# Kernel tuning notes

Measured on AMD Instinct MI355X. Metric: run time of the kernel, lower is better.

## Reference

```python
import jax, jax.numpy as jnp
import numpy as np

V, H, L, B = 32000, 1024, 2, 64
TEMP = 0.8


def setup_inputs() -> dict:
    key = jax.random.key(0)
    ks = jax.random.split(key, 12)
    sV = 1.0 / np.sqrt(V)
    sH = 1.0 / np.sqrt(H)
    return {
        "x": jax.random.normal(ks[0], (B, V), jnp.float32),
        "hidden_states": jax.random.normal(ks[1], (L, B, H), jnp.float32),
        "cell_states": jax.random.normal(ks[2], (L, B, H), jnp.float32),
        # gate order along axis 1: f, i, o, g
        "Wh": jax.random.uniform(ks[3], (L, 4, H, H), jnp.float32, -sH, sH),
        "bh": jax.random.uniform(ks[4], (L, 4, H), jnp.float32, -sH, sH),
        "Wx0": jax.random.uniform(ks[5], (4, H, V), jnp.float32, -sV, sV),
        "bx0": jax.random.uniform(ks[6], (4, H), jnp.float32, -sV, sV),
        "Wx1": jax.random.uniform(ks[7], (4, H, H), jnp.float32, -sH, sH),
        "bx1": jax.random.uniform(ks[8], (4, H), jnp.float32, -sH, sH),
        "Wdec": jax.random.uniform(ks[9], (V, H), jnp.float32, -sH, sH),
        "bdec": jax.random.uniform(ks[10], (V,), jnp.float32, -sH, sH),
    }


def _lstm_cell(inp, h, c, Wx, bx, Whl, bhl):
    # fused gate pre-activations: [B, 4, H]
    z = (jnp.einsum("ghk,bk->bgh", Wx, inp) + bx[None]
         + jnp.einsum("ghk,bk->bgh", Whl, h) + bhl[None])
    f = jax.nn.sigmoid(z[:, 0])
    i = jax.nn.sigmoid(z[:, 1])
    o = jax.nn.sigmoid(z[:, 2])
    g = jnp.tanh(z[:, 3])
    c_new = f * c + i * g
    out = o * jnp.tanh(c_new)
    return out, c_new


def reference(x, hidden_states, cell_states, Wh, bh, Wx0, bx0, Wx1, bx1, Wdec, bdec):
    wx = [(Wx0, bx0), (Wx1, bx1)]
    outputs, cstates = [], []
    inp = x
    for l in range(L):
        out, c_new = _lstm_cell(inp, hidden_states[l], cell_states[l],
                                wx[l][0], wx[l][1], Wh[l], bh[l])
        outputs.append(out)
        cstates.append(c_new)
        inp = out
    logits = outputs[-1] @ Wdec.T + bdec
    logp = jax.nn.log_softmax(logits / TEMP, axis=-1)
    return logp, jnp.stack(outputs), jnp.stack(cstates)
```

## Files before the change

### kernel.cpp

```cpp
#include <hip/hip_runtime.h>
#include <hip/hip_bf16.h>
#include <cstdint>

#define DI __device__ __forceinline__

typedef __attribute__((ext_vector_type(8))) short short8;
typedef __attribute__((ext_vector_type(4))) float f32x4;
typedef __attribute__((ext_vector_type(4))) int int4v;

DI f32x4 mfma16(short8 a, short8 b, f32x4 c) {
  return __builtin_amdgcn_mfma_f32_16x16x32_bf16(a, b, c, 0, 0, 0);
}

DI uint32_t f2bf(float f) {
  uint32_t u = __float_as_uint(f);
  return (u + 0x7fffu + ((u >> 16) & 1u)) >> 16;
}

DI uint32_t pk2(float a, float b) {
  return f2bf(a) | (f2bf(b) << 16);
}

DI short8 cvt8(float4 a, float4 b) {
  int4v t;
  t.x = (int)pk2(a.x, a.y);
  t.y = (int)pk2(a.z, a.w);
  t.z = (int)pk2(b.x, b.y);
  t.w = (int)pk2(b.z, b.w);
  return __builtin_bit_cast(short8, t);
}

__global__ __launch_bounds__(256) void convert_k(
    const float* __restrict__ x, const float* __restrict__ hs,
    ushort* __restrict__ xb, ushort* __restrict__ hb) {
  const int NX4 = 512000;
  const int NH4 = 32768;
  int i = blockIdx.x * 256 + threadIdx.x;
  if (i < NX4) {
    float4 v = *(const float4*)(x + 4 * (size_t)i);
    uint2 o;
    o.x = pk2(v.x, v.y);
    o.y = pk2(v.z, v.w);
    *(uint2*)(xb + 4 * (size_t)i) = o;
  } else if (i < NX4 + NH4) {
    int j = i - NX4;
    float4 v = *(const float4*)(hs + 4 * (size_t)j);
    uint2 o;
    o.x = pk2(v.x, v.y);
    o.y = pk2(v.z, v.w);
    *(uint2*)(hb + 4 * (size_t)j) = o;
  }
}

__global__ __launch_bounds__(256, 2) void gates_pf(
    const ushort* __restrict__ xb, const ushort* __restrict__ hb,
    const float* __restrict__ Wx0, const float* __restrict__ Wh,
    float* __restrict__ zpart) {
  const int y = blockIdx.y;
  const ushort* A;
  const float* W;
  int ldA, K, steps;
  long kbase;
  if (y < 25) {
    A = xb; ldA = 32000; W = Wx0; K = 32000; steps = 20;
    kbase = (long)y * 1280;
  } else if (y < 27) {
    A = hb; ldA = 1024; W = Wh; K = 1024; steps = 8;
    kbase = (long)(y - 25) * 512;
  } else {
    A = hb + 65536; ldA = 1024; W = Wh + 4194304; K = 1024; steps = 8;
    kbase = (long)(y - 27) * 512;
  }
  const int tid = threadIdx.x;
  const int wv = tid >> 6;
  const int lane = tid & 63;
  const int l15 = lane & 15;
  const int l4 = lane >> 4;
  const int h = blockIdx.x * 64 + wv * 16 + l15;

  const ushort* arow[4];
#pragma unroll
  for (int m = 0; m < 4; ++m)
    arow[m] = A + (size_t)(m * 16 + l15) * ldA + kbase + l4 * 8;
  const float* wrow[4];
#pragma unroll
  for (int g = 0; g < 4; ++g)
    wrow[g] = W + (size_t)(g * 1024 + h) * K + kbase + l4 * 8;

  f32x4 acc[4][4];
#pragma unroll
  for (int g = 0; g < 4; ++g)
#pragma unroll
    for (int m = 0; m < 4; ++m)
      acc[g][m] = f32x4{0.f, 0.f, 0.f, 0.f};

  float4 wt[4][4];
  short8 wb0[4], wb1[4];

#pragma unroll
  for (int g = 0; g < 4; ++g) {
    const float* wp = wrow[g];
    wt[g][0] = *(const float4*)wp;
    wt[g][1] = *(const float4*)(wp + 4);
    wt[g][2] = *(const float4*)(wp + 32);
    wt[g][3] = *(const float4*)(wp + 36);
  }
#pragma unroll
  for (int g = 0; g < 4; ++g) {
    wb0[g] = cvt8(wt[g][0], wt[g][1]);
    wb1[g] = cvt8(wt[g][2], wt[g][3]);
  }

  for (int s = 0; s < steps; ++s) {
    short8 af0[4], af1[4];
#pragma unroll
    for (int m = 0; m < 4; ++m) {
      const ushort* ap = arow[m] + (size_t)s * 64;
      af0[m] = *(const short8*)ap;
      af1[m] = *(const short8*)(ap + 32);
    }
    if (s + 1 < steps) {
#pragma unroll
      for (int g = 0; g < 4; ++g) {
        const float* wp = wrow[g] + (size_t)(s + 1) * 64;
        wt[g][0] = *(const float4*)wp;
        wt[g][1] = *(const float4*)(wp + 4);
        wt[g][2] = *(const float4*)(wp + 32);
        wt[g][3] = *(const float4*)(wp + 36);
      }
    }
#pragma unroll
    for (int g = 0; g < 4; ++g)
#pragma unroll
      for (int m = 0; m < 4; ++m) {
        acc[g][m] = mfma16(af0[m], wb0[g], acc[g][m]);
        acc[g][m] = mfma16(af1[m], wb1[g], acc[g][m]);
      }
    if (s + 1 < steps) {
#pragma unroll
      for (int g = 0; g < 4; ++g) {
        wb0[g] = cvt8(wt[g][0], wt[g][1]);
        wb1[g] = cvt8(wt[g][2], wt[g][3]);
      }
    }
  }

  float* zp = zpart + (size_t)y * 262144 + (size_t)(l4 * 4) * 4096 + h;
#pragma unroll
  for (int g = 0; g < 4; ++g)
#pragma unroll
    for (int m = 0; m < 4; ++m)
#pragma unroll
      for (int r = 0; r < 4; ++r)
        zp[(size_t)(m * 16 + r) * 4096 + g * 1024] = acc[g][m][r];
}

__global__ __launch_bounds__(256) void gates_b16(
    const ushort* __restrict__ A, const float* __restrict__ W,
    float* __restrict__ zbase) {
  const int chunk = blockIdx.y;
  const long kbase = (long)chunk * 64;
  const int tid = threadIdx.x;
  const int wv = tid >> 6;
  const int lane = tid & 63;
  const int l15 = lane & 15;
  const int l4 = lane >> 4;
  const int h = blockIdx.x * 64 + wv * 16 + l15;

  const ushort* arow[4];
#pragma unroll
  for (int m = 0; m < 4; ++m)
    arow[m] = A + (size_t)(m * 16 + l15) * 1024 + kbase + l4 * 8;
  const float* wrow[4];
#pragma unroll
  for (int g = 0; g < 4; ++g)
    wrow[g] = W + (size_t)(g * 1024 + h) * 1024 + kbase + l4 * 8;

  f32x4 acc[4][4];
#pragma unroll
  for (int g = 0; g < 4; ++g)
#pragma unroll
    for (int m = 0; m < 4; ++m)
      acc[g][m] = f32x4{0.f, 0.f, 0.f, 0.f};

#pragma unroll
  for (int s = 0; s < 2; ++s) {
    short8 af[4];
#pragma unroll
    for (int m = 0; m < 4; ++m)
      af[m] = *(const short8*)(arow[m] + (size_t)s * 32);
#pragma unroll
    for (int g = 0; g < 4; ++g) {
      const float* wp = wrow[g] + (size_t)s * 32;
      float4 w0 = *(const float4*)wp;
      float4 w1 = *(const float4*)(wp + 4);
      short8 bfr = cvt8(w0, w1);
#pragma unroll
      for (int m = 0; m < 4; ++m)
        acc[g][m] = mfma16(af[m], bfr, acc[g][m]);
    }
  }

  float* zp = zbase + (size_t)chunk * 262144 + (size_t)(l4 * 4) * 4096 + h;
#pragma unroll
  for (int g = 0; g < 4; ++g)
#pragma unroll
    for (int m = 0; m < 4; ++m)
#pragma unroll
      for (int r = 0; r < 4; ++r)
        zp[(size_t)(m * 16 + r) * 4096 + g * 1024] = acc[g][m][r];
}

__global__ __launch_bounds__(256) void lstm_cell_k(
    const float* __restrict__ zpart, int nslots,
    const float* __restrict__ bx, const float* __restrict__ bhl,
    const float* __restrict__ c_in,
    float* __restrict__ h_out, float* __restrict__ c_out,
    ushort* __restrict__ h_out_b) {
  int idx = blockIdx.x * 256 + threadIdx.x;
  if (idx >= 64 * 1024) return;
  int h = idx & 1023;
  float z0 = bx[h] + bhl[h];
  float z1 = bx[1024 + h] + bhl[1024 + h];
  float z2 = bx[2048 + h] + bhl[2048 + h];
  float z3 = bx[3072 + h] + bhl[3072 + h];
  int b = idx >> 10;
  const float* zp = zpart + (size_t)b * 4096 + h;
  for (int s = 0; s < nslots; ++s) {
    const float* p = zp + (size_t)s * 262144;
    z0 += p[0];
    z1 += p[1024];
    z2 += p[2048];
    z3 += p[3072];
  }
  float f = 1.f / (1.f + expf(-z0));
  float i = 1.f / (1.f + expf(-z1));
  float o = 1.f / (1.f + expf(-z2));
  float g = tanhf(z3);
  float c = f * c_in[idx] + i * g;
  float hv = o * tanhf(c);
  h_out[idx] = hv;
  c_out[idx] = c;
  h_out_b[idx] = (ushort)f2bf(hv);
}

__global__ __launch_bounds__(64) void gemm_dec(
    const ushort* __restrict__ A, const float* __restrict__ W,
    const float* __restrict__ bias, float* __restrict__ logits) {
  const int lane = threadIdx.x;
  const int l15 = lane & 15;
  const int l4 = lane >> 4;
  const int col = blockIdx.x * 16 + l15;

  const ushort* arow[4];
#pragma unroll
  for (int m = 0; m < 4; ++m)
    arow[m] = A + (size_t)(m * 16 + l15) * 1024 + l4 * 8;
  const float* wrow = W + (size_t)col * 1024 + l4 * 8;

  f32x4 acc[4];
#pragma unroll
  for (int m = 0; m < 4; ++m) acc[m] = f32x4{0.f, 0.f, 0.f, 0.f};

  for (int s = 0; s < 32; ++s) {
    short8 af[4];
#pragma unroll
    for (int m = 0; m < 4; ++m)
      af[m] = *(const short8*)(arow[m] + (size_t)s * 32);
    const float* wp = wrow + (size_t)s * 32;
    float4 w0 = *(const float4*)wp;
    float4 w1 = *(const float4*)(wp + 4);
    short8 bfr = cvt8(w0, w1);
#pragma unroll
    for (int m = 0; m < 4; ++m)
      acc[m] = mfma16(af[m], bfr, acc[m]);
  }

  float bv = bias[col];
  float* lp = logits + (size_t)(l4 * 4) * 32000 + col;
#pragma unroll
  for (int m = 0; m < 4; ++m)
#pragma unroll
    for (int r = 0; r < 4; ++r)
      lp[(size_t)(m * 16 + r) * 32000] = acc[m][r] + bv;
}

__global__ __launch_bounds__(256) void softmax_part1(
    const float* __restrict__ logits, float2* __restrict__ ms) {
  const int cx = blockIdx.x;
  const int b = blockIdx.y;
  const int tid = threadIdx.x;
  const int wv = tid >> 6;
  const int lane = tid & 63;
  const float* row = logits + (size_t)b * 32000 + cx * 8000;
  __shared__ float rbuf[4];

  float m = -1e30f;
  for (int i = tid; i < 8000; i += 256) m = fmaxf(m, row[i]);
#pragma unroll
  for (int d = 1; d < 64; d <<= 1) m = fmaxf(m, __shfl_xor(m, d));
  if (lane == 0) rbuf[wv] = m;
  __syncthreads();
  m = fmaxf(fmaxf(rbuf[0], rbuf[1]), fmaxf(rbuf[2], rbuf[3]));
  __syncthreads();

  float sum = 0.f;
  for (int i = tid; i < 8000; i += 256) sum += expf((row[i] - m) * 1.25f);
#pragma unroll
  for (int d = 1; d < 64; d <<= 1) sum += __shfl_xor(sum, d);
  if (lane == 0) rbuf[wv] = sum;
  __syncthreads();
  if (tid == 0) {
    sum = rbuf[0] + rbuf[1] + rbuf[2] + rbuf[3];
    ms[b * 4 + cx] = make_float2(m, sum);
  }
}

__global__ __launch_bounds__(256) void softmax_part2(
    const float* __restrict__ logits, const float2* __restrict__ ms,
    float* __restrict__ logp) {
  const int cx = blockIdx.x;
  const int b = blockIdx.y;
  const int tid = threadIdx.x;

  float2 p0 = ms[b * 4 + 0], p1 = ms[b * 4 + 1];
  float2 p2 = ms[b * 4 + 2], p3 = ms[b * 4 + 3];
  float M = fmaxf(fmaxf(p0.x, p1.x), fmaxf(p2.x, p3.x));
  float S = p0.y * expf((p0.x - M) * 1.25f) + p1.y * expf((p1.x - M) * 1.25f) +
            p2.y * expf((p2.x - M) * 1.25f) + p3.y * expf((p3.x - M) * 1.25f);
  float lse = logf(S);

  const float* row = logits + (size_t)b * 32000 + cx * 4000;
  float* op = logp + (size_t)b * 32000 + cx * 4000;
  for (int i = tid; i < 4000; i += 256)
    op[i] = (row[i] - M) * 1.25f - lse;
}

extern "C" void kernel_launch(void* const* d_in, const int* in_sizes, int n_in,
                              void* d_out, int out_size, void* d_ws, size_t ws_size,
                              hipStream_t stream) {
  const float* x    = (const float*)d_in[0];
  const float* hs   = (const float*)d_in[1];
  const float* cs   = (const float*)d_in[2];
  const float* Wh   = (const float*)d_in[3];
  const float* bh   = (const float*)d_in[4];
  const float* Wx0  = (const float*)d_in[5];
  const float* bx0  = (const float*)d_in[6];
  const float* Wx1  = (const float*)d_in[7];
  const float* bx1  = (const float*)d_in[8];
  const float* Wdec = (const float*)d_in[9];
  const float* bdec = (const float*)d_in[10];

  float* out   = (float*)d_out;
  float* logp  = out;
  float* houts = out + 2048000;
  float* couts = out + 2179072;

  char* ws = (char*)d_ws;
  ushort* xb     = (ushort*)ws;
  ushort* hb     = (ushort*)(ws + 4096000);
  ushort* outb   = (ushort*)(ws + 4358144);
  float*  logits = (float*)(ws + 4620288);
  float2* ms     = (float2*)(ws + 12812288);
  float*  zpart  = (float*)(ws + 12814336);

  convert_k<<<2128, 256, 0, stream>>>(x, hs, xb, hb);

  gates_pf<<<dim3(16, 29), 256, 0, stream>>>(xb, hb, Wx0, Wh, zpart);

  lstm_cell_k<<<256, 256, 0, stream>>>(zpart, 27, bx0, bh, cs,
                                       houts, couts, outb);

  gates_b16<<<dim3(16, 16), 256, 0, stream>>>(
      outb, Wx1, zpart + (size_t)29 * 262144);

  lstm_cell_k<<<256, 256, 0, stream>>>(zpart + (size_t)27 * 262144, 18,
                                       bx1, bh + 4096, cs + 65536,
                                       houts + 65536, couts + 65536,
                                       outb + 65536);

  gemm_dec<<<2000, 64, 0, stream>>>(outb + 65536, Wdec, bdec, logits);

  softmax_part1<<<dim3(4, 64), 256, 0, stream>>>(logits, ms);
  softmax_part2<<<dim3(8, 64), 256, 0, stream>>>(logits, ms, logp);
}
```

Before: 280.6 us.

## Split gate dimension across grid z and double-buffer weight prefetch in gates kernel

```diff
diff --git a/kernel.cpp b/kernel.cpp
--- a/kernel.cpp
+++ b/kernel.cpp
@@ -52,11 +52,12 @@
   }
 }
 
-__global__ __launch_bounds__(256, 2) void gates_pf(
+__global__ __launch_bounds__(256, 2) void gates_pf2(
     const ushort* __restrict__ xb, const ushort* __restrict__ hb,
     const float* __restrict__ Wx0, const float* __restrict__ Wh,
     float* __restrict__ zpart) {
   const int y = blockIdx.y;
+  const int gz = blockIdx.z;
   const ushort* A;
   const float* W;
   int ldA, K, steps;
@@ -82,77 +83,71 @@
 #pragma unroll
   for (int m = 0; m < 4; ++m)
     arow[m] = A + (size_t)(m * 16 + l15) * ldA + kbase + l4 * 8;
-  const float* wrow[4];
-#pragma unroll
-  for (int g = 0; g < 4; ++g)
-    wrow[g] = W + (size_t)(g * 1024 + h) * K + kbase + l4 * 8;
-
-  f32x4 acc[4][4];
-#pragma unroll
-  for (int g = 0; g < 4; ++g)
-#pragma unroll
-    for (int m = 0; m < 4; ++m)
-      acc[g][m] = f32x4{0.f, 0.f, 0.f, 0.f};
-
-  float4 wt[4][4];
-  short8 wb0[4], wb1[4];
-
-#pragma unroll
-  for (int g = 0; g < 4; ++g) {
-    const float* wp = wrow[g];
-    wt[g][0] = *(const float4*)wp;
-    wt[g][1] = *(const float4*)(wp + 4);
-    wt[g][2] = *(const float4*)(wp + 32);
-    wt[g][3] = *(const float4*)(wp + 36);
-  }
-#pragma unroll
-  for (int g = 0; g < 4; ++g) {
-    wb0[g] = cvt8(wt[g][0], wt[g][1]);
-    wb1[g] = cvt8(wt[g][2], wt[g][3]);
-  }
-
-  for (int s = 0; s < steps; ++s) {
-    short8 af0[4], af1[4];
-#pragma unroll
-    for (int m = 0; m < 4; ++m) {
-      const ushort* ap = arow[m] + (size_t)s * 64;
-      af0[m] = *(const short8*)ap;
-      af1[m] = *(const short8*)(ap + 32);
-    }
-    if (s + 1 < steps) {
-#pragma unroll
-      for (int g = 0; g < 4; ++g) {
-        const float* wp = wrow[g] + (size_t)(s + 1) * 64;
-        wt[g][0] = *(const float4*)wp;
-        wt[g][1] = *(const float4*)(wp + 4);
-        wt[g][2] = *(const float4*)(wp + 32);
-        wt[g][3] = *(const float4*)(wp + 36);
-      }
-    }
-#pragma unroll
-    for (int g = 0; g < 4; ++g)
-#pragma unroll
-      for (int m = 0; m < 4; ++m) {
-        acc[g][m] = mfma16(af0[m], wb0[g], acc[g][m]);
-        acc[g][m] = mfma16(af1[m], wb1[g], acc[g][m]);
-      }
-    if (s + 1 < steps) {
-#pragma unroll
-      for (int g = 0; g < 4; ++g) {
-        wb0[g] = cvt8(wt[g][0], wt[g][1]);
-        wb1[g] = cvt8(wt[g][2], wt[g][3]);
-      }
-    }
-  }
-
-  float* zp = zpart + (size_t)y * 262144 + (size_t)(l4 * 4) * 4096 + h;
-#pragma unroll
-  for (int g = 0; g < 4; ++g)
+  const float* wrow[2];
+#pragma unroll
+  for (int gi = 0; gi < 2; ++gi)
+    wrow[gi] = W + (size_t)((gz * 2 + gi) * 1024 + h) * K + kbase + l4 * 8;
+
+  f32x4 acc[2][4];
+#pragma unroll
+  for (int gi = 0; gi < 2; ++gi)
+#pragma unroll
+    for (int m = 0; m < 4; ++m)
+      acc[gi][m] = f32x4{0.f, 0.f, 0.f, 0.f};
+
+  float4 wtA[2][4], wtB[2][4];
+
+#define LOADW(dst, ss)                                             \
+  {                                                                \
+    _Pragma("unroll") for (int gi = 0; gi < 2; ++gi) {             \
+      const float* wp = wrow[gi] + (size_t)(ss) * 64;              \
+      dst[gi][0] = *(const float4*)wp;                             \
+      dst[gi][1] = *(const float4*)(wp + 4);                       \
+      dst[gi][2] = *(const float4*)(wp + 32);                      \
+      dst[gi][3] = *(const float4*)(wp + 36);                      \
+    }                                                              \
+  }
+
+#define SUBITER(wt, ss, reload_s)                                  \
+  {                                                                \
+    short8 af0[4], af1[4];                                         \
+    _Pragma("unroll") for (int m = 0; m < 4; ++m) {                \
+      const ushort* ap = arow[m] + (size_t)(ss) * 64;              \
+      af0[m] = *(const short8*)ap;                                 \
+      af1[m] = *(const short8*)(ap + 32);                          \
+    }                                                              \
+    short8 wb0[2], wb1[2];                                         \
+    _Pragma("unroll") for (int gi = 0; gi < 2; ++gi) {             \
+      wb0[gi] = cvt8(wt[gi][0], wt[gi][1]);                        \
+      wb1[gi] = cvt8(wt[gi][2], wt[gi][3]);                        \
+    }                                                              \
+    if ((reload_s) < steps) LOADW(wt, (reload_s));                 \
+    _Pragma("unroll") for (int gi = 0; gi < 2; ++gi)               \
+        _Pragma("unroll") for (int m = 0; m < 4; ++m) {            \
+      acc[gi][m] = mfma16(af0[m], wb0[gi], acc[gi][m]);            \
+      acc[gi][m] = mfma16(af1[m], wb1[gi], acc[gi][m]);            \
+    }                                                              \
+  }
+
+  LOADW(wtA, 0);
+  LOADW(wtB, 1);
+
+  for (int s = 0; s < steps; s += 2) {
+    SUBITER(wtA, s, s + 2);
+    SUBITER(wtB, s + 1, s + 3);
+  }
+#undef SUBITER
+#undef LOADW
+
+  float* zp = zpart + (size_t)y * 262144 + (size_t)(l4 * 4) * 4096 +
+              (gz * 2) * 1024 + h;
+#pragma unroll
+  for (int gi = 0; gi < 2; ++gi)
 #pragma unroll
     for (int m = 0; m < 4; ++m)
 #pragma unroll
       for (int r = 0; r < 4; ++r)
-        zp[(size_t)(m * 16 + r) * 4096 + g * 1024] = acc[g][m][r];
+        zp[(size_t)(m * 16 + r) * 4096 + gi * 1024] = acc[gi][m][r];
 }
 
 __global__ __launch_bounds__(256) void gates_b16(
@@ -366,7 +361,7 @@
 
   convert_k<<<2128, 256, 0, stream>>>(x, hs, xb, hb);
 
-  gates_pf<<<dim3(16, 29), 256, 0, stream>>>(xb, hb, Wx0, Wh, zpart);
+  gates_pf2<<<dim3(16, 29, 2), 256, 0, stream>>>(xb, hb, Wx0, Wh, zpart);
 
   lstm_cell_k<<<256, 256, 0, stream>>>(zpart, 27, bx0, bh, cs,
                                        houts, couts, outb);
```

New measurement: 277.1 us. About the same (-1.3%).
